# Kernel tuning notes

Hardware: AMD Instinct MI355X
Metric: run time of the kernel (lower is better)

The kernel has to match this reference:

```python
import jax, jax.numpy as jnp
from jax import lax
import numpy as np

C = 256; NH = 8; NP = 4; FFN = 512; B = 2; H = 128; W = 128
HD = C // NH


def _ln(x, g, b):
    m = jnp.mean(x, -1, keepdims=True)
    v = jnp.var(x, -1, keepdims=True)
    return (x - m) * lax.rsqrt(v + 1e-5) * g + b


def _deform_attn(q, kv, off_w, off_b, attw_w, attw_b, vp_w, vp_b, op_w, op_b):
    # q, kv: (B, N, C) with N = H*W
    Bn, N, Cc = q.shape
    val = (kv @ vp_w + vp_b).reshape(Bn, N, NH, HD)
    off = (q @ off_w + off_b).reshape(Bn, N, NH, NP, 2)
    attw = jax.nn.softmax((q @ attw_w + attw_b).reshape(Bn, N, NH, NP), axis=-1)
    # identity-grid reference points (normalized, pixel centers)
    ry = (jnp.arange(H, dtype=q.dtype) + 0.5) / H
    rx = (jnp.arange(W, dtype=q.dtype) + 0.5) / W
    gy, gx = jnp.meshgrid(ry, rx, indexing='ij')
    ref = jnp.stack([gx.ravel(), gy.ravel()], -1)  # (N, 2) as (x, y)
    norm = jnp.array([W, H], dtype=q.dtype)
    loc = ref[None, :, None, None, :] + off / norm  # (B,N,NH,NP,2) in [0,1]
    # grid_sample align_corners=False, zeros padding
    x = loc[..., 0] * W - 0.5
    y = loc[..., 1] * H - 0.5
    x0 = jnp.floor(x); y0 = jnp.floor(y)
    lx = x - x0; ly = y - y0
    x0i = x0.astype(jnp.int32); y0i = y0.astype(jnp.int32)
    v_t = val.transpose(0, 2, 1, 3)  # (B, NH, N, HD)

    def gather(xi, yi, w):
        valid = (xi >= 0) & (xi < W) & (yi >= 0) & (yi < H)
        idx = jnp.clip(yi, 0, H - 1) * W + jnp.clip(xi, 0, W - 1)  # (B,N,NH,NP)
        idx_t = idx.transpose(0, 2, 1, 3).reshape(Bn, NH, N * NP)
        g = jnp.take_along_axis(v_t, idx_t[..., None], axis=2)
        g = g.reshape(Bn, NH, N, NP, HD)
        wm = (w * valid).transpose(0, 2, 1, 3)  # (B,NH,N,NP)
        return g * wm[..., None]

    samp = (gather(x0i, y0i, (1 - lx) * (1 - ly))
            + gather(x0i + 1, y0i, lx * (1 - ly))
            + gather(x0i, y0i + 1, (1 - lx) * ly)
            + gather(x0i + 1, y0i + 1, lx * ly))  # (B,NH,N,NP,HD)
    out = jnp.einsum('bhnpd,bnhp->bnhd', samp, attw).reshape(Bn, N, Cc)
    return out @ op_w + op_b


def _forward(cam_bev, sat_bev,
             c2s_off_w, c2s_off_b, c2s_attw_w, c2s_attw_b, c2s_vp_w, c2s_vp_b, c2s_op_w, c2s_op_b,
             s2c_off_w, s2c_off_b, s2c_attw_w, s2c_attw_b, s2c_vp_w, s2c_vp_b, s2c_op_w, s2c_op_b,
             ln1_g, ln1_b, ln2_g, ln2_b, lnf_g, lnf_b,
             ffn1_w, ffn1_b, ffn2_w, ffn2_b,
             g1_w, bn_g, bn_b, g2_w, g2_b):
    Bn, Cc, Hh, Ww = cam_bev.shape
    q_cam = cam_bev.reshape(Bn, Cc, Hh * Ww).transpose(0, 2, 1)
    q_sat = sat_bev.reshape(Bn, Cc, Hh * Ww).transpose(0, 2, 1)
    c2s = _deform_attn(q_cam, q_sat, c2s_off_w, c2s_off_b, c2s_attw_w, c2s_attw_b,
                       c2s_vp_w, c2s_vp_b, c2s_op_w, c2s_op_b)
    cam_att = _ln(q_cam + c2s, ln1_g, ln1_b)
    s2c = _deform_attn(q_sat, q_cam, s2c_off_w, s2c_off_b, s2c_attw_w, s2c_attw_b,
                       s2c_vp_w, s2c_vp_b, s2c_op_w, s2c_op_b)
    sat_att = _ln(q_sat + s2c, ln2_g, ln2_b)
    cam_map = cam_att.transpose(0, 2, 1).reshape(Bn, Cc, Hh, Ww)
    sat_map = sat_att.transpose(0, 2, 1).reshape(Bn, Cc, Hh, Ww)
    gi = jnp.concatenate([cam_map, sat_map], axis=1)
    h = lax.conv_general_dilated(gi, g1_w, (1, 1), 'SAME',
                                 dimension_numbers=('NCHW', 'OIHW', 'NCHW'))
    # BatchNorm2d in eval mode: running_mean=0, running_var=1
    h = jax.nn.relu(h * lax.rsqrt(jnp.float32(1.0 + 1e-5)) * bn_g[None, :, None, None]
                    + bn_b[None, :, None, None])
    g = jax.nn.sigmoid(jnp.einsum('bchw,oc->bohw', h, g2_w) + g2_b[None, :, None, None])
    fused = g * cam_map + (1 - g) * sat_map
    ff = fused.reshape(Bn, Cc, Hh * Ww).transpose(0, 2, 1)
    ff = ff + (jax.nn.relu(ff @ ffn1_w + ffn1_b) @ ffn2_w + ffn2_b)
    ff = _ln(ff, lnf_g, lnf_b)
    return ff.transpose(0, 2, 1).reshape(Bn, Cc, Hh, Ww) + cam_bev


def setup_inputs() -> dict:
    key = jax.random.key(0)
    ks = iter(jax.random.split(key, 40))

    def rn(shape, s=0.02):
        return jax.random.normal(next(ks), shape, jnp.float32) * s

    # directional offset-bias init (as in original init_weights)
    thetas = np.arange(NH) * (2.0 * np.pi / NH)
    grid = np.stack([np.cos(thetas), np.sin(thetas)], -1)
    grid = grid / np.abs(grid).max(-1, keepdims=True)
    grid = np.tile(grid[:, None, :], (1, NP, 1)) * np.arange(1, NP + 1)[None, :, None]
    off_bias = jnp.asarray(grid.reshape(-1), jnp.float32)

    def attn_params():
        return dict(off_w=rn((C, NH * NP * 2), 0.01), off_b=off_bias,
                    attw_w=rn((C, NH * NP), 0.02), attw_b=rn((NH * NP,), 0.02),
                    vp_w=rn((C, C), 0.05), vp_b=jnp.zeros((C,), jnp.float32),
                    op_w=rn((C, C), 0.05), op_b=jnp.zeros((C,), jnp.float32))

    p1 = attn_params(); p2 = attn_params()
    inp = {
        'cam_bev': jax.random.normal(next(ks), (B, C, H, W), jnp.float32),
        'sat_bev': jax.random.normal(next(ks), (B, C, H, W), jnp.float32),
    }
    for pre, p in (('c2s_', p1), ('s2c_', p2)):
        for k, v in p.items():
            inp[pre + k] = v
    inp.update(
        ln1_g=jnp.ones((C,), jnp.float32), ln1_b=jnp.zeros((C,), jnp.float32),
        ln2_g=jnp.ones((C,), jnp.float32), ln2_b=jnp.zeros((C,), jnp.float32),
        lnf_g=jnp.ones((C,), jnp.float32), lnf_b=jnp.zeros((C,), jnp.float32),
        ffn1_w=rn((C, FFN), 0.05), ffn1_b=jnp.zeros((FFN,), jnp.float32),
        ffn2_w=rn((FFN, C), 0.05), ffn2_b=jnp.zeros((C,), jnp.float32),
        g1_w=rn((C // 2, 2 * C, 3, 3), 0.02),
        bn_g=jnp.ones((C // 2,), jnp.float32), bn_b=jnp.zeros((C // 2,), jnp.float32),
        g2_w=rn((C, C // 2), 0.02), g2_b=jnp.zeros((C,), jnp.float32),
    )
    return inp


def reference(cam_bev, sat_bev,
              c2s_off_w, c2s_off_b, c2s_attw_w, c2s_attw_b, c2s_vp_w, c2s_vp_b, c2s_op_w, c2s_op_b,
              s2c_off_w, s2c_off_b, s2c_attw_w, s2c_attw_b, s2c_vp_w, s2c_vp_b, s2c_op_w, s2c_op_b,
              ln1_g, ln1_b, ln2_g, ln2_b, lnf_g, lnf_b,
              ffn1_w, ffn1_b, ffn2_w, ffn2_b,
              g1_w, bn_g, bn_b, g2_w, g2_b):
    return _forward(cam_bev, sat_bev,
                    c2s_off_w, c2s_off_b, c2s_attw_w, c2s_attw_b, c2s_vp_w, c2s_vp_b, c2s_op_w, c2s_op_b,
                    s2c_off_w, s2c_off_b, s2c_attw_w, s2c_attw_b, s2c_vp_w, s2c_vp_b, s2c_op_w, s2c_op_b,
                    ln1_g, ln1_b, ln2_g, ln2_b, lnf_g, lnf_b,
                    ffn1_w, ffn1_b, ffn2_w, ffn2_b,
                    g1_w, bn_g, bn_b, g2_w, g2_b)
```

## Files before the change

kernel.cpp:

```cpp
#include <hip/hip_runtime.h>
#include <hip/hip_bf16.h>
#include <cstddef>

#define BBn  2
#define CCn  256
#define HHn  128
#define WWn  128
#define NNn  (HHn*WWn)
#define MTOT (BBn*NNn)
#define PADW 130

typedef unsigned short u16;
typedef __attribute__((ext_vector_type(8))) short bf8v;
typedef __attribute__((ext_vector_type(8))) unsigned short u16x8;
typedef __attribute__((ext_vector_type(4))) float f4v;

typedef __attribute__((address_space(1))) const void gvoid_t;
typedef __attribute__((address_space(3))) void svoid_t;
#define ASYNC16(g, l) __builtin_amdgcn_global_load_lds((gvoid_t*)(g), (svoid_t*)(l), 16, 0, 0)

__device__ __forceinline__ u16 f2bf(float f) {
    __hip_bfloat16 h = __float2bfloat16(f);
    return *reinterpret_cast<u16*>(&h);
}
__device__ __forceinline__ float bf2f(u16 h) {
    return __uint_as_float(((unsigned)h) << 16);
}

struct ZOff {
    long a, w, bia, f1, f2, b1, r, p;
    int ch;
};

template<int BM, int BN, int WC, int EPI, int KK>
__global__ __launch_bounds__(256)
void mgemm(const u16* __restrict__ A, const u16* __restrict__ Wt,
           const float* __restrict__ bias, int ldw, int Nc,
           float* __restrict__ outf, float* __restrict__ outf2,
           u16* __restrict__ outb, const u16* __restrict__ img,
           const void* __restrict__ resid,
           const float* __restrict__ p0, const float* __restrict__ p1,
           int choff, ZOff zo)
{
    constexpr int WR = 4 / WC;
    constexpr int MROWS = BM / WR;
    constexpr int MI = MROWS / 16;
    constexpr int AT = BM / 64;
    constexpr int BT = BN / 64;

    __shared__ __align__(16) u16 As[BM * 32];
    __shared__ __align__(16) u16 Bs[BN * 32];
    __shared__ float red[4][64][2];

    const int z = blockIdx.z;
    if (z) {
        A += (long)z * zo.a; Wt += (long)z * zo.w;
        if (bias)  bias  += (long)z * zo.bia;
        if (outf)  outf  += (long)z * zo.f1;
        if (outf2) outf2 += (long)z * zo.f2;
        if (outb)  outb  += (long)z * zo.b1;
        if (p0)    p0    += (long)z * zo.p;
        if (p1)    p1    += (long)z * zo.p;
        choff += z * zo.ch;
    }

    const int tid  = threadIdx.x;
    const int lane = tid & 63;
    const int w    = tid >> 6;
    const int wr   = w / WC, wc = w % WC;
    const int by = blockIdx.y;
    const int m0 = by * BM;
    const int n0 = blockIdx.x * BN;
    const int lr = lane & 15, lq = lane >> 4;
    const int kb = lq * 8;

    const u16* gA[AT];
    #pragma unroll
    for (int t = 0; t < AT; ++t) {
        int c = t * 256 + tid; int row = c >> 2; int part = c & 3;
        gA[t] = A + (size_t)(m0 + row) * KK + part * 8;
    }
    const u16* gB[BT];
    #pragma unroll
    for (int t = 0; t < BT; ++t) {
        int c = t * 256 + tid; int row = c >> 2; int part = c & 3;
        gB[t] = Wt + (size_t)(n0 + row) * ldw + part * 8;
    }

    f4v acc[MI][4];
    if constexpr (EPI == 7 || EPI == 9) {
        const u16* r16 = (const u16*)resid + (EPI == 7 ? (long)z * zo.r : 0);
        #pragma unroll
        for (int j = 0; j < 4; ++j) {
            int n = wc * 64 + j * 16 + lr;
            float bj = bias[n];
            #pragma unroll
            for (int i = 0; i < MI; ++i)
                #pragma unroll
                for (int r = 0; r < 4; ++r) {
                    int m = m0 + i * 16 + lq * 4 + r;
                    acc[i][j][r] = bf2f(r16[(size_t)m * 256 + n]) + bj;
                }
        }
    } else {
        #pragma unroll
        for (int i = 0; i < MI; ++i)
            #pragma unroll
            for (int j = 0; j < 4; ++j)
                acc[i][j] = (f4v){0.f, 0.f, 0.f, 0.f};
    }

    for (int k0 = 0; k0 < KK; k0 += 32) {
        #pragma unroll
        for (int t = 0; t < AT; ++t)
            ASYNC16(gA[t] + k0, (u16*)As + (t * 256 + tid) * 8);
        #pragma unroll
        for (int t = 0; t < BT; ++t)
            ASYNC16(gB[t] + k0, (u16*)Bs + (t * 256 + tid) * 8);
        __syncthreads();

        bf8v af[MI], bv[4];
        #pragma unroll
        for (int i = 0; i < MI; ++i)
            af[i] = *(const bf8v*)&As[(wr * MROWS + i * 16 + lr) * 32 + kb];
        #pragma unroll
        for (int j = 0; j < 4; ++j)
            bv[j] = *(const bf8v*)&Bs[(wc * 64 + j * 16 + lr) * 32 + kb];
        #pragma unroll
        for (int i = 0; i < MI; ++i)
            #pragma unroll
            for (int j = 0; j < 4; ++j)
                acc[i][j] = __builtin_amdgcn_mfma_f32_16x16x32_bf16(af[i], bv[j], acc[i][j], 0, 0, 0);
        __syncthreads();
    }

    if constexpr (EPI == 7 || EPI == 9) {
        float g4[4], b4[4];
        #pragma unroll
        for (int j = 0; j < 4; ++j) {
            int n = wc * 64 + j * 16 + lr;
            g4[j] = p0[n]; b4[j] = p1[n];
        }
        #pragma unroll
        for (int i = 0; i < MI; ++i)
            #pragma unroll
            for (int r = 0; r < 4; ++r) {
                float p = 0.f, p2 = 0.f;
                #pragma unroll
                for (int j = 0; j < 4; ++j) { float v = acc[i][j][r]; p += v; p2 += v * v; }
                p += __shfl_xor(p, 1, 16);  p2 += __shfl_xor(p2, 1, 16);
                p += __shfl_xor(p, 2, 16);  p2 += __shfl_xor(p2, 2, 16);
                p += __shfl_xor(p, 4, 16);  p2 += __shfl_xor(p2, 4, 16);
                p += __shfl_xor(p, 8, 16);  p2 += __shfl_xor(p2, 8, 16);
                if (lr == 0) {
                    int row = i * 16 + lq * 4 + r;
                    red[w][row][0] = p; red[w][row][1] = p2;
                }
            }
        __syncthreads();
        #pragma unroll
        for (int i = 0; i < MI; ++i) {
            float mean4[4], rstd4[4];
            #pragma unroll
            for (int r = 0; r < 4; ++r) {
                int row = i * 16 + lq * 4 + r;
                float s  = red[0][row][0] + red[1][row][0] + red[2][row][0] + red[3][row][0];
                float s2 = red[0][row][1] + red[1][row][1] + red[2][row][1] + red[3][row][1];
                float mean = s * (1.f / 256.f);
                float var  = s2 * (1.f / 256.f) - mean * mean;
                mean4[r] = mean;
                rstd4[r] = rsqrtf(var + 1e-5f);
            }
            if constexpr (EPI == 7) {
                #pragma unroll
                for (int r = 0; r < 4; ++r) {
                    int m = m0 + i * 16 + lq * 4 + r;
                    int b = m >> 14, sp = m & (NNn - 1);
                    size_t pb = (((size_t)b * PADW + (sp >> 7) + 1) * PADW + (sp & 127) + 1) * 512 + choff;
                    #pragma unroll
                    for (int j = 0; j < 4; ++j) {
                        int n = wc * 64 + j * 16 + lr;
                        outb[pb + n] = f2bf((acc[i][j][r] - mean4[r]) * rstd4[r] * g4[j] + b4[j]);
                    }
                }
            } else {
                int mb = m0 + i * 16 + lq * 4;
                int b = mb >> 14, sp = mb & (NNn - 1);
                #pragma unroll
                for (int j = 0; j < 4; ++j) {
                    int n = wc * 64 + j * 16 + lr;
                    size_t oi = ((size_t)b * 256 + n) * NNn + sp;
                    float4 cv = *(const float4*)&outf2[oi];
                    float4 o;
                    o.x = (acc[i][j][0] - mean4[0]) * rstd4[0] * g4[j] + b4[j] + cv.x;
                    o.y = (acc[i][j][1] - mean4[1]) * rstd4[1] * g4[j] + b4[j] + cv.y;
                    o.z = (acc[i][j][2] - mean4[2]) * rstd4[2] * g4[j] + b4[j] + cv.z;
                    o.w = (acc[i][j][3] - mean4[3]) * rstd4[3] * g4[j] + b4[j] + cv.w;
                    *(float4*)&outf[oi] = o;
                }
            }
        }
        return;
    }

    float bj[4]; int ncol[4];
    #pragma unroll
    for (int j = 0; j < 4; ++j) {
        int n = n0 + wc * 64 + j * 16 + lr;
        ncol[j] = n;
        if constexpr (EPI == 0 || EPI == 4 || EPI == 5) bj[j] = bias[n];
    }
    #pragma unroll
    for (int i = 0; i < MI; ++i) {
        #pragma unroll
        for (int r = 0; r < 4; ++r) {
            int m = m0 + wr * MROWS + i * 16 + lq * 4 + r;
            size_t pb = 0;
            if constexpr (EPI == 4) {
                int b = m >> 14, sp = m & (NNn - 1);
                pb = (((size_t)b * PADW + (sp >> 7) + 1) * PADW + (sp & 127) + 1) * 512;
            }
            #pragma unroll
            for (int j = 0; j < 4; ++j) {
                int n = ncol[j];
                float v = acc[i][j][r];
                size_t oi = (size_t)m * Nc + n;
                if constexpr (EPI == 0) {
                    outb[oi] = f2bf(v + bj[j]);
                } else if constexpr (EPI == 2) {
                    if (n < 64)      outf [(size_t)m * 64 + n]        = v + p0[n];
                    else if (n < 96) outf2[(size_t)m * 32 + (n - 64)] = v + p1[n - 64];
                } else if constexpr (EPI == 4) {
                    float vv = v + bj[j];
                    float g = 1.f / (1.f + __expf(-vv));
                    float f = g * bf2f(img[pb + n]) + (1.f - g) * bf2f(img[pb + 256 + n]);
                    outb[oi] = f2bf(f);
                } else if constexpr (EPI == 5) {
                    outb[oi] = f2bf(fmaxf(v + bj[j], 0.f));
                }
            }
        }
    }
}

template<int TAPS>
__global__ __launch_bounds__(256)
void conv_k(const u16* __restrict__ img, const u16* __restrict__ Wt,
            float* __restrict__ outp)
{
    __shared__ __align__(16) u16 As[128 * 64];
    __shared__ __align__(16) u16 Bs[128 * 64];

    const int z = blockIdx.z;
    outp += (size_t)z * MTOT * 128;
    const int tid = threadIdx.x;
    const int lane = tid & 63;
    const int w = tid >> 6;
    const int wr = w >> 1, wc = w & 1;
    int by = blockIdx.y;
    by = ((by & 7) << 5) | (by >> 3);
    const int m0 = by * 128;
    const int lr = lane & 15, lq = lane >> 4;

    long cbA[4]; int pgA[4]; const u16* wB[4]; int ldsOff[4];
    #pragma unroll
    for (int t = 0; t < 4; ++t) {
        int c = t * 256 + tid;
        int row = c >> 3, part = c & 7;
        int pg = part ^ (row & 7);
        ldsOff[t] = c * 8;
        int m = m0 + row; int b = m >> 14; int sp = m & (NNn - 1);
        cbA[t] = ((long)b * PADW + (sp >> 7)) * PADW + (sp & 127);
        pgA[t] = pg;
        wB[t] = Wt + (size_t)row * 4608 + pg * 8;
    }

    f4v acc[4][4];
    #pragma unroll
    for (int i = 0; i < 4; ++i)
        #pragma unroll
        for (int j = 0; j < 4; ++j)
            acc[i][j] = (f4v){0.f, 0.f, 0.f, 0.f};

    const int tap0 = z * TAPS;
    #pragma unroll
    for (int tt = 0; tt < TAPS; ++tt) {
        int tap = tap0 + tt;
        int dy = tap / 3, dx = tap - dy * 3;
        const u16* bpA[4]; const u16* bpB[4];
        #pragma unroll
        for (int t = 0; t < 4; ++t) {
            bpA[t] = img + (size_t)(cbA[t] + dy * PADW + dx) * 512 + pgA[t] * 8;
            bpB[t] = wB[t] + tap * 512;
        }
        #pragma unroll 2
        for (int ci = 0; ci < 512; ci += 64) {
            #pragma unroll
            for (int t = 0; t < 4; ++t)
                ASYNC16(bpA[t] + ci, (u16*)As + ldsOff[t]);
            #pragma unroll
            for (int t = 0; t < 4; ++t)
                ASYNC16(bpB[t] + ci, (u16*)Bs + ldsOff[t]);
            __syncthreads();
            #pragma unroll
            for (int kk = 0; kk < 2; ++kk) {
                bf8v af[4], bv[4];
                #pragma unroll
                for (int i = 0; i < 4; ++i) {
                    int row = wr * 64 + i * 16 + lr;
                    af[i] = *(const bf8v*)&As[(row * 8 + ((kk * 4 + lq) ^ (row & 7))) * 8];
                }
                #pragma unroll
                for (int j = 0; j < 4; ++j) {
                    int row = wc * 64 + j * 16 + lr;
                    bv[j] = *(const bf8v*)&Bs[(row * 8 + ((kk * 4 + lq) ^ (row & 7))) * 8];
                }
                #pragma unroll
                for (int i = 0; i < 4; ++i)
                    #pragma unroll
                    for (int j = 0; j < 4; ++j)
                        acc[i][j] = __builtin_amdgcn_mfma_f32_16x16x32_bf16(af[i], bv[j], acc[i][j], 0, 0, 0);
            }
            __syncthreads();
        }
    }

    #pragma unroll
    for (int i = 0; i < 4; ++i)
        #pragma unroll
        for (int r = 0; r < 4; ++r) {
            int m = m0 + wr * 64 + i * 16 + lq * 4 + r;
            #pragma unroll
            for (int j = 0; j < 4; ++j) {
                int n = wc * 64 + j * 16 + lr;
                outp[(size_t)m * 128 + n] = acc[i][j][r];
            }
        }
}

__global__ __launch_bounds__(256)
void combine_k(const float* __restrict__ part, const float* __restrict__ bng,
               const float* __restrict__ bnb, u16* __restrict__ hb)
{
    const float bnscale = rsqrtf(1.0f + 1e-5f);
    int i = (blockIdx.x * 256 + threadIdx.x) * 4;
    int n = i & 127;
    float4 a = *(const float4*)&part[i];
    float4 b = *(const float4*)&part[(size_t)MTOT * 128 + i];
    float4 c = *(const float4*)&part[(size_t)MTOT * 256 + i];
    ushort4 o;
    o.x = f2bf(fmaxf((a.x + b.x + c.x) * bnscale * bng[n + 0] + bnb[n + 0], 0.f));
    o.y = f2bf(fmaxf((a.y + b.y + c.y) * bnscale * bng[n + 1] + bnb[n + 1], 0.f));
    o.z = f2bf(fmaxf((a.z + b.z + c.z) * bnscale * bng[n + 2] + bnb[n + 2], 0.f));
    o.w = f2bf(fmaxf((a.w + b.w + c.w) * bnscale * bng[n + 3] + bnb[n + 3], 0.f));
    *(ushort4*)&hb[i] = o;
}

__global__ __launch_bounds__(256)
void tcvt_k(const float* __restrict__ cam, const float* __restrict__ sat,
            u16* __restrict__ qcam, u16* __restrict__ qsat)
{
    __shared__ float t[64][65];
    int z = blockIdx.z;
    const float* src = (z < 2) ? cam : sat;
    u16* dst = (z < 2) ? qcam : qsat;
    int b = z & 1;
    int c0 = blockIdx.x * 64, sp0 = blockIdx.y * 64;
    #pragma unroll
    for (int it = 0; it < 16; ++it) {
        int idx = it * 256 + threadIdx.x;
        int cl = idx >> 6, sl = idx & 63;
        t[cl][sl] = src[((size_t)(b * CCn + c0 + cl)) * NNn + sp0 + sl];
    }
    __syncthreads();
    #pragma unroll
    for (int it = 0; it < 16; ++it) {
        int idx = it * 256 + threadIdx.x;
        int sl = idx >> 6, cl = idx & 63;
        dst[((size_t)(b * NNn + sp0 + sl)) * CCn + c0 + cl] = f2bf(t[cl][sl]);
    }
}

__global__ __launch_bounds__(256)
void sample_k(const u16* __restrict__ val, const float* __restrict__ off,
              const float* __restrict__ lg, u16* __restrict__ outp)
{
    int z = blockIdx.z;
    val  += (size_t)z * MTOT * CCn;
    off  += (size_t)z * MTOT * 64;
    lg   += (size_t)z * MTOT * 32;
    outp += (size_t)z * MTOT * CCn;

    int t = blockIdx.x * 256 + threadIdx.x;
    int h  = t & 7;
    int rn = t >> 3;
    int n = rn & (NNn - 1), b = rn >> 14;
    int yp = n >> 7, xp = n & 127;

    const float* ofp = off + (size_t)rn * 64 + h * 8;
    const float* lgp = lg  + (size_t)rn * 32 + h * 4;

    float4 of0 = *(const float4*)ofp;
    float4 of1 = *(const float4*)(ofp + 4);
    float4 lgv = *(const float4*)lgp;
    float ofx[4] = { of0.x, of0.z, of1.x, of1.z };
    float ofy[4] = { of0.y, of0.w, of1.y, of1.w };

    float mx = fmaxf(fmaxf(lgv.x, lgv.y), fmaxf(lgv.z, lgv.w));
    float e0 = __expf(lgv.x - mx), e1 = __expf(lgv.y - mx);
    float e2 = __expf(lgv.z - mx), e3 = __expf(lgv.w - mx);
    float inv = 1.f / (e0 + e1 + e2 + e3);
    float aw[4] = { e0 * inv, e1 * inv, e2 * inv, e3 * inv };

    const u16* vb = val + (size_t)b * NNn * CCn + h * 32;
    float acc[32];
    #pragma unroll
    for (int q = 0; q < 32; ++q) acc[q] = 0.f;

    #pragma unroll
    for (int p = 0; p < 4; ++p) {
        float xs = (float)xp + ofx[p];
        float ys = (float)yp + ofy[p];
        float x0f = floorf(xs), y0f = floorf(ys);
        float lx = xs - x0f, ly = ys - y0f;
        int x0 = (int)x0f, y0 = (int)y0f;
        #pragma unroll
        for (int c = 0; c < 4; ++c) {
            int xi = x0 + (c & 1), yi = y0 + (c >> 1);
            float wgt = aw[p] * ((c & 1) ? lx : 1.f - lx) * ((c >> 1) ? ly : 1.f - ly);
            if (xi >= 0 && xi < WWn && yi >= 0 && yi < HHn) {
                const u16* src = vb + (size_t)(yi * WWn + xi) * CCn;
                #pragma unroll
                for (int q = 0; q < 4; ++q) {
                    u16x8 v = *(const u16x8*)(src + q * 8);
                    #pragma unroll
                    for (int e = 0; e < 8; ++e)
                        acc[q * 8 + e] += wgt * bf2f(v[e]);
                }
            }
        }
    }

    u16* dst = outp + (size_t)rn * CCn + h * 32;
    #pragma unroll
    for (int q = 0; q < 4; ++q) {
        u16x8 o;
        #pragma unroll
        for (int e = 0; e < 8; ++e) o[e] = f2bf(acc[q * 8 + e]);
        *(u16x8*)(dst + q * 8) = o;
    }
}

__global__ __launch_bounds__(256)
void repack_all(const float* __restrict__ vp1, const float* __restrict__ op1,
                const float* __restrict__ vp2, const float* __restrict__ op2,
                const float* __restrict__ f1w, const float* __restrict__ f2w,
                const float* __restrict__ of1, const float* __restrict__ aw1,
                const float* __restrict__ of2, const float* __restrict__ aw2,
                const float* __restrict__ g1,  const float* __restrict__ g2,
                const float* __restrict__ vpb1, const float* __restrict__ vpb2,
                const float* __restrict__ opb1, const float* __restrict__ opb2,
                const float* __restrict__ ofb1, const float* __restrict__ awb1,
                const float* __restrict__ ofb2, const float* __restrict__ awb2,
                const float* __restrict__ l1g, const float* __restrict__ l1b,
                const float* __restrict__ l2g, const float* __restrict__ l2b,
                u16* __restrict__ wb, float* __restrict__ bb)
{
    int i = blockIdx.x * 256 + threadIdx.x;
    if (i >= 1212416 + 2240) return;
    if (i >= 1212416) {
        int j = i - 1212416;
        float v;
        if      (j < 256)  v = vpb1[j];
        else if (j < 512)  v = vpb2[j - 256];
        else if (j < 768)  v = opb1[j - 512];
        else if (j < 1024) v = opb2[j - 768];
        else if (j < 1088) v = ofb1[j - 1024];
        else if (j < 1120) v = awb1[j - 1088];
        else if (j < 1184) v = ofb2[j - 1120];
        else if (j < 1216) v = awb2[j - 1184];
        else if (j < 1472) v = l1g[j - 1216];
        else if (j < 1728) v = l1b[j - 1472];
        else if (j < 1984) v = l2g[j - 1728];
        else               v = l2b[j - 1984];
        bb[j] = v;
        return;
    }
    float v;
    if (i < 262144) {
        const float* src[4] = { vp1, vp2, op1, op2 };
        int q = i >> 16, j = i & 65535;
        int n = j >> 8, k = j & 255;
        v = src[q][(size_t)k * 256 + n];
    } else if (i < 393216) {
        int j = i - 262144; int n = j >> 8, k = j & 255;
        v = f1w[(size_t)k * 512 + n];
    } else if (i < 524288) {
        int j = i - 393216; int n = j >> 9, k = j & 511;
        v = f2w[(size_t)k * 256 + n];
    } else if (i < 589824) {
        int jj = i - 524288; int hh = jj >> 15; int j = jj & 32767;
        int n = j >> 8, k = j & 255;
        const float* ofw = hh ? of2 : of1;
        const float* aww = hh ? aw2 : aw1;
        if (n < 64)      v = ofw[(size_t)k * 64 + n];
        else if (n < 96) v = aww[(size_t)k * 32 + (n - 64)];
        else             v = 0.f;
    } else if (i < 1179648) {
        int j = i - 589824; int co = j / 4608, k = j - co * 4608;
        int tap = k >> 9, ci = k & 511;
        v = g1[((size_t)co * 512 + ci) * 9 + tap];
    } else {
        int j = i - 1179648; int n = j >> 7, k = j & 127;
        v = g2[(size_t)n * 128 + k];
    }
    wb[i] = f2bf(v);
}

extern "C" void kernel_launch(void* const* d_in, const int* in_sizes, int n_in,
                              void* d_out, int out_size, void* d_ws, size_t ws_size,
                              hipStream_t stream)
{
    const float* cam_bev   = (const float*)d_in[0];
    const float* sat_bev   = (const float*)d_in[1];
    const float* c2s_off_w  = (const float*)d_in[2];
    const float* c2s_off_b  = (const float*)d_in[3];
    const float* c2s_attw_w = (const float*)d_in[4];
    const float* c2s_attw_b = (const float*)d_in[5];
    const float* c2s_vp_w   = (const float*)d_in[6];
    const float* c2s_vp_b   = (const float*)d_in[7];
    const float* c2s_op_w   = (const float*)d_in[8];
    const float* c2s_op_b   = (const float*)d_in[9];
    const float* s2c_off_w  = (const float*)d_in[10];
    const float* s2c_off_b  = (const float*)d_in[11];
    const float* s2c_attw_w = (const float*)d_in[12];
    const float* s2c_attw_b = (const float*)d_in[13];
    const float* s2c_vp_w   = (const float*)d_in[14];
    const float* s2c_vp_b   = (const float*)d_in[15];
    const float* s2c_op_w   = (const float*)d_in[16];
    const float* s2c_op_b   = (const float*)d_in[17];
    const float* ln1_g = (const float*)d_in[18];
    const float* ln1_b = (const float*)d_in[19];
    const float* ln2_g = (const float*)d_in[20];
    const float* ln2_b = (const float*)d_in[21];
    const float* lnf_g = (const float*)d_in[22];
    const float* lnf_b = (const float*)d_in[23];
    const float* ffn1_w = (const float*)d_in[24];
    const float* ffn1_b = (const float*)d_in[25];
    const float* ffn2_w = (const float*)d_in[26];
    const float* ffn2_b = (const float*)d_in[27];
    const float* g1_w  = (const float*)d_in[28];
    const float* bn_g  = (const float*)d_in[29];
    const float* bn_b  = (const float*)d_in[30];
    const float* g2_w  = (const float*)d_in[31];
    const float* g2_b  = (const float*)d_in[32];

    char* base = (char*)d_ws;
    size_t off = 0;
    auto alloc = [&](size_t bytes) -> void* {
        void* p = base + off;
        off += (bytes + 255) & ~(size_t)255;
        return p;
    };

    u16*   qcam   = (u16*)  alloc((size_t)MTOT * CCn * 2 * 2);
    u16*   qsat   = qcam + (size_t)MTOT * CCn;
    u16*   valb   = (u16*)  alloc((size_t)MTOT * CCn * 2 * 2);
    u16*   sampb  = (u16*)  alloc((size_t)MTOT * CCn * 2 * 2);
    float* offb   = (float*)alloc((size_t)MTOT * 64 * 4 * 2);
    float* attwb  = (float*)alloc((size_t)MTOT * 32 * 4 * 2);
    size_t padBytes = (size_t)BBn * PADW * PADW * 512 * 2;
    u16*   pad    = (u16*)  alloc(padBytes);
    u16*   hbuf   = (u16*)  alloc((size_t)MTOT * 128 * 2);
    u16*   wbase  = (u16*)  alloc((size_t)1212416 * 2);
    float* biasbf = (float*)alloc((size_t)2240 * 4);
    u16* wvp = wbase;
    u16* wop = wbase + 131072;
    u16* wf1 = wbase + 262144;
    u16* wf2 = wbase + 393216;
    u16* woa = wbase + 524288;
    u16* wcv = wbase + 589824;
    u16* wg2 = wbase + 1179648;
    u16*   fused_bf = valb;
    float* convpart = (float*)sampb;
    u16*   midb     = qcam;

    dim3 blk(256);
    ZOff zz{0, 0, 0, 0, 0, 0, 0, 0, 0};

    hipMemsetAsync(pad, 0, padBytes, stream);
    tcvt_k<<<dim3(4, 256, 4), blk, 0, stream>>>(cam_bev, sat_bev, qcam, qsat);
    repack_all<<<4746, blk, 0, stream>>>(c2s_vp_w, c2s_op_w, s2c_vp_w, s2c_op_w,
                                         ffn1_w, ffn2_w, c2s_off_w, c2s_attw_w,
                                         s2c_off_w, s2c_attw_w, g1_w, g2_w,
                                         c2s_vp_b, s2c_vp_b, c2s_op_b, s2c_op_b,
                                         c2s_off_b, c2s_attw_b, s2c_off_b, s2c_attw_b,
                                         ln1_g, ln1_b, ln2_g, ln2_b,
                                         wbase, biasbf);

    {
        ZOff zo{ -(long)MTOT * CCn, 65536, 256, 0, 0, (long)MTOT * CCn, 0, 0, 0 };
        mgemm<128, 128, 2, 0, 256><<<dim3(2, 256, 2), blk, 0, stream>>>(
            qsat, wvp, biasbf, 256, 256,
            nullptr, nullptr, valb, nullptr, nullptr, nullptr, nullptr, 0, zo);
    }
    {
        ZOff zo{ (long)MTOT * CCn, 32768, 0, (long)MTOT * 64, (long)MTOT * 32, 0, 0, 96, 0 };
        mgemm<128, 128, 2, 2, 256><<<dim3(1, 256, 2), blk, 0, stream>>>(
            qcam, woa, nullptr, 256, 128,
            offb, attwb, nullptr, nullptr, nullptr, biasbf + 1024, biasbf + 1088, 0, zo);
    }
    sample_k<<<dim3(1024, 1, 2), blk, 0, stream>>>(valb, offb, attwb, sampb);
    {
        ZOff zo{ (long)MTOT * CCn, 65536, 256, 0, 0, 0, (long)MTOT * CCn, 512, 256 };
        mgemm<64, 256, 4, 7, 256><<<dim3(1, 512, 2), blk, 0, stream>>>(
            sampb, wop, biasbf + 512, 256, 256,
            nullptr, nullptr, pad, nullptr, qcam, biasbf + 1216, biasbf + 1472, 0, zo);
    }
    conv_k<3><<<dim3(1, 256, 3), blk, 0, stream>>>(pad, wcv, convpart);
    combine_k<<<4096, blk, 0, stream>>>(convpart, bn_g, bn_b, hbuf);

    mgemm<128, 128, 2, 4, 128><<<dim3(2, 256, 1), blk, 0, stream>>>(
        hbuf, wg2, g2_b, 128, 256,
        nullptr, nullptr, fused_bf, pad, nullptr, nullptr, nullptr, 0, zz);

    mgemm<128, 128, 2, 5, 256><<<dim3(4, 256, 1), blk, 0, stream>>>(
        fused_bf, wf1, ffn1_b, 256, 512,
        nullptr, nullptr, midb, nullptr, nullptr, nullptr, nullptr, 0, zz);
    mgemm<64, 256, 4, 9, 512><<<dim3(1, 512, 1), blk, 0, stream>>>(
        midb, wf2, ffn2_b, 512, 256,
        (float*)d_out, (float*)cam_bev, nullptr, nullptr, fused_bf, lnf_g, lnf_b, 0, zz);
}
```

Baseline: 322.6 us.

## Split deformable sampling into descriptor stage and 8-lane coalesced gather

The sampling kernel is reorganized. First, 32 threads per block compute the bilinear addresses and weights for each (pixel, head) pair and store them in a shared-memory descriptor table. Then all 256 threads gather: 8 threads cooperate on one head's 32 channels with 8-byte loads, instead of one thread loading all 32 channels per corner. This raises parallelism eightfold, makes the gather loads coalesced, and replaces the divergent bounds branch with clamped addresses and zero weights. The cost is a sync per block, idle lanes during the descriptor phase, and more blocks.

```diff
diff --git a/kernel.cpp b/kernel.cpp
--- a/kernel.cpp
+++ b/kernel.cpp
@@ -385,70 +385,80 @@
 void sample_k(const u16* __restrict__ val, const float* __restrict__ off,
               const float* __restrict__ lg, u16* __restrict__ outp)
 {
+    __shared__ uint2 desc[32][17];
+
     int z = blockIdx.z;
     val  += (size_t)z * MTOT * CCn;
     off  += (size_t)z * MTOT * 64;
     lg   += (size_t)z * MTOT * 32;
     outp += (size_t)z * MTOT * CCn;
 
-    int t = blockIdx.x * 256 + threadIdx.x;
-    int h  = t & 7;
-    int rn = t >> 3;
-    int n = rn & (NNn - 1), b = rn >> 14;
-    int yp = n >> 7, xp = n & 127;
-
-    const float* ofp = off + (size_t)rn * 64 + h * 8;
-    const float* lgp = lg  + (size_t)rn * 32 + h * 4;
-
-    float4 of0 = *(const float4*)ofp;
-    float4 of1 = *(const float4*)(ofp + 4);
-    float4 lgv = *(const float4*)lgp;
-    float ofx[4] = { of0.x, of0.z, of1.x, of1.z };
-    float ofy[4] = { of0.y, of0.w, of1.y, of1.w };
-
-    float mx = fmaxf(fmaxf(lgv.x, lgv.y), fmaxf(lgv.z, lgv.w));
-    float e0 = __expf(lgv.x - mx), e1 = __expf(lgv.y - mx);
-    float e2 = __expf(lgv.z - mx), e3 = __expf(lgv.w - mx);
-    float inv = 1.f / (e0 + e1 + e2 + e3);
-    float aw[4] = { e0 * inv, e1 * inv, e2 * inv, e3 * inv };
-
-    const u16* vb = val + (size_t)b * NNn * CCn + h * 32;
-    float acc[32];
-    #pragma unroll
-    for (int q = 0; q < 32; ++q) acc[q] = 0.f;
-
-    #pragma unroll
-    for (int p = 0; p < 4; ++p) {
-        float xs = (float)xp + ofx[p];
-        float ys = (float)yp + ofy[p];
-        float x0f = floorf(xs), y0f = floorf(ys);
-        float lx = xs - x0f, ly = ys - y0f;
-        int x0 = (int)x0f, y0 = (int)y0f;
-        #pragma unroll
-        for (int c = 0; c < 4; ++c) {
-            int xi = x0 + (c & 1), yi = y0 + (c >> 1);
-            float wgt = aw[p] * ((c & 1) ? lx : 1.f - lx) * ((c >> 1) ? ly : 1.f - ly);
-            if (xi >= 0 && xi < WWn && yi >= 0 && yi < HHn) {
-                const u16* src = vb + (size_t)(yi * WWn + xi) * CCn;
-                #pragma unroll
-                for (int q = 0; q < 4; ++q) {
-                    u16x8 v = *(const u16x8*)(src + q * 8);
-                    #pragma unroll
-                    for (int e = 0; e < 8; ++e)
-                        acc[q * 8 + e] += wgt * bf2f(v[e]);
-                }
-            }
-        }
-    }
-
-    u16* dst = outp + (size_t)rn * CCn + h * 32;
-    #pragma unroll
-    for (int q = 0; q < 4; ++q) {
-        u16x8 o;
-        #pragma unroll
-        for (int e = 0; e < 8; ++e) o[e] = f2bf(acc[q * 8 + e]);
-        *(u16x8*)(dst + q * 8) = o;
-    }
+    const int tid = threadIdx.x;
+    const int rh0 = blockIdx.x * 32;
+
+    if (tid < 32) {
+        int rhg = rh0 + tid;
+        int h = rhg & 7, rn = rhg >> 3;
+        int n = rn & (NNn - 1), b = rn >> 14;
+        int yp = n >> 7, xp = n & 127;
+
+        const float* ofp = off + (size_t)rn * 64 + h * 8;
+        const float* lgp = lg  + (size_t)rn * 32 + h * 4;
+        float4 of0 = *(const float4*)ofp;
+        float4 of1 = *(const float4*)(ofp + 4);
+        float4 lgv = *(const float4*)lgp;
+        float ofx[4] = { of0.x, of0.z, of1.x, of1.z };
+        float ofy[4] = { of0.y, of0.w, of1.y, of1.w };
+
+        float mx = fmaxf(fmaxf(lgv.x, lgv.y), fmaxf(lgv.z, lgv.w));
+        float e0 = __expf(lgv.x - mx), e1 = __expf(lgv.y - mx);
+        float e2 = __expf(lgv.z - mx), e3 = __expf(lgv.w - mx);
+        float inv = 1.f / (e0 + e1 + e2 + e3);
+        float aw[4] = { e0 * inv, e1 * inv, e2 * inv, e3 * inv };
+
+        unsigned hb = (unsigned)(b * NNn) * 256u + h * 32;
+        #pragma unroll
+        for (int p = 0; p < 4; ++p) {
+            float xs = (float)xp + ofx[p];
+            float ys = (float)yp + ofy[p];
+            float x0f = floorf(xs), y0f = floorf(ys);
+            float lx = xs - x0f, ly = ys - y0f;
+            int x0 = (int)x0f, y0 = (int)y0f;
+            #pragma unroll
+            for (int c = 0; c < 4; ++c) {
+                int xi = x0 + (c & 1), yi = y0 + (c >> 1);
+                bool valid = (xi >= 0) & (xi < WWn) & (yi >= 0) & (yi < HHn);
+                float wgt = valid
+                    ? aw[p] * ((c & 1) ? lx : 1.f - lx) * ((c >> 1) ? ly : 1.f - ly)
+                    : 0.f;
+                int xc = min(max(xi, 0), WWn - 1);
+                int yc = min(max(yi, 0), HHn - 1);
+                unsigned addr = hb + (unsigned)(yc * WWn + xc) * 256u;
+                desc[tid][p * 4 + c] = make_uint2(addr, __float_as_uint(wgt));
+            }
+        }
+    }
+    __syncthreads();
+
+    const int rh = tid >> 3;
+    const int q  = tid & 7;
+    const int rhg = rh0 + rh;
+    const int h = rhg & 7, rn = rhg >> 3;
+
+    float a0 = 0.f, a1 = 0.f, a2 = 0.f, a3 = 0.f;
+    #pragma unroll
+    for (int k = 0; k < 16; ++k) {
+        uint2 d = desc[rh][k];
+        float wgt = __uint_as_float(d.y);
+        ushort4 v = *(const ushort4*)(val + d.x + q * 4);
+        a0 += wgt * bf2f(v.x);
+        a1 += wgt * bf2f(v.y);
+        a2 += wgt * bf2f(v.z);
+        a3 += wgt * bf2f(v.w);
+    }
+    ushort4 o;
+    o.x = f2bf(a0); o.y = f2bf(a1); o.z = f2bf(a2); o.w = f2bf(a3);
+    *(ushort4*)(outp + (size_t)rn * CCn + h * 32 + q * 4) = o;
 }
 
 __global__ __launch_bounds__(256)
@@ -610,7 +620,7 @@
             qcam, woa, nullptr, 256, 128,
             offb, attwb, nullptr, nullptr, nullptr, biasbf + 1024, biasbf + 1088, 0, zo);
     }
-    sample_k<<<dim3(1024, 1, 2), blk, 0, stream>>>(valb, offb, attwb, sampb);
+    sample_k<<<dim3(8192, 1, 2), blk, 0, stream>>>(valb, offb, attwb, sampb);
     {
         ZOff zo{ (long)MTOT * CCn, 65536, 256, 0, 0, 0, (long)MTOT * CCn, 512, 256 };
         mgemm<64, 256, 4, 7, 256><<<dim3(1, 512, 2), blk, 0, stream>>>(
```

Measured after the change: 306.0 us. 5.2% less time.
